# Optimization experiments

Measured on AMD Instinct MI355X. Metric: run time of the kernel, lower is better.

The kernel has to match this reference:

```python
import jax, jax.numpy as jnp
import numpy as np

B, C_IN, C_OUT, D, H, W = 2, 128, 128, 16, 32, 32


def setup_inputs() -> dict:
    key = jax.random.key(0)
    kx, kw, kb = jax.random.split(key, 3)
    x = jax.random.normal(kx, (B, C_IN, D, H, W), dtype=jnp.float32)
    # ddpm_conv3x3 -> Conv3d(in_ch, out_ch, kernel=3, padding=1) with default (scaled-variance) init
    fan_in = C_IN * 3 * 3 * 3
    scale = 1.0 / np.sqrt(fan_in)
    Wk = jax.random.uniform(kw, (C_OUT, C_IN, 3, 3, 3), dtype=jnp.float32, minval=-scale, maxval=scale)
    b = jnp.zeros((C_OUT,), dtype=jnp.float32)
    return {"x": x, "Wk": Wk, "b": b}


def reference(x, Wk, b):
    h = jnp.repeat(jnp.repeat(jnp.repeat(x, 2, axis=2), 2, axis=3), 2, axis=4)
    # 3x3x3 conv, stride 1, padding 1 (SAME)
    out = jax.lax.conv_general_dilated(
        h, Wk,
        window_strides=(1, 1, 1),
        padding="SAME",
        dimension_numbers=("NCDHW", "OIDHW", "NCDHW"),
    )
    return out + b[None, :, None, None, None]
```

## Files before the change

kernel.cpp:

```cpp
#include <hip/hip_runtime.h>
#include <hip/hip_bf16.h>

#define B_    2
#define CIN   128
#define COUT  128
#define DD    16
#define HH    32
#define WW    32
#define XS_CI (DD*HH*WW)
#define XS_B  (CIN*XS_CI)
#define OS_H2 64
#define OS_D2 (64*64)
#define OS_CO (32*64*64)
#define OS_B  (COUT*OS_CO)

#define PD_D  18
#define PD_H  34
#define PD_W  36
#define PD_HW (PD_H*PD_W)
#define PD_CI (PD_D*PD_HW)
#define AFOLD_BYTES (8*32*8*64*16)
#define XPAD_ELEMS  ((size_t)B_*CIN*PD_CI)
#define XPAD_BYTES  (XPAD_ELEMS*2)

typedef __attribute__((ext_vector_type(8))) short        short8;
typedef __attribute__((ext_vector_type(4))) float        floatx4;
typedef __attribute__((ext_vector_type(4))) unsigned int uint4v;

static __device__ __forceinline__ unsigned f2bf(float f) {
    union { __hip_bfloat16 h; unsigned short u; } cv;
    cv.h = __float2bfloat16(f);
    return (unsigned)cv.u;
}

__global__ __launch_bounds__(256) void fold_kernel(const float* __restrict__ Wk,
                                                   unsigned short* __restrict__ Afold) {
    const int t = blockIdx.x * 256 + threadIdx.x;
    const int p  = t >> 14;
    const int ks = (t >> 9) & 31;
    const int ct = (t >> 6) & 7;
    const int l  = t & 63;
    const int co = ct * 16 + (l & 15);
    const int ci = ks * 4 + (l >> 4);
    const int ed = (p >> 2) & 1, eh = (p >> 1) & 1, ew = p & 1;

    const float* w = Wk + (co * CIN + ci) * 27;
    float wv[27];
    #pragma unroll
    for (int i = 0; i < 27; ++i) wv[i] = w[i];

    short8 pk;
    #pragma unroll
    for (int tt = 0; tt < 8; ++tt) {
        const int td = (tt >> 2) & 1, th = (tt >> 1) & 1, tw = tt & 1;
        const int dlo = ed ? (td ? 2 : 0) : (td ? 1 : 0);
        const int dhi = ed ? (td ? 2 : 1) : (td ? 2 : 0);
        const int hlo = eh ? (th ? 2 : 0) : (th ? 1 : 0);
        const int hhi = eh ? (th ? 2 : 1) : (th ? 2 : 0);
        const int wlo = ew ? (tw ? 2 : 0) : (tw ? 1 : 0);
        const int whi = ew ? (tw ? 2 : 1) : (tw ? 2 : 0);
        float s = 0.f;
        for (int kd = dlo; kd <= dhi; ++kd)
            for (int kh = hlo; kh <= hhi; ++kh)
                for (int kw = wlo; kw <= whi; ++kw)
                    s += wv[kd * 9 + kh * 3 + kw];
        pk[tt] = (short)f2bf(s);
    }
    reinterpret_cast<short8*>(Afold)[t] = pk;
}

__global__ __launch_bounds__(256) void pad_kernel(const float* __restrict__ x,
                                                  unsigned* __restrict__ xp32) {
    const int idx = blockIdx.x * 256 + threadIdx.x;
    const int w2 = idx & 15;
    const int h  = (idx >> 4) & 31;
    const int d  = (idx >> 9) & 15;
    const int ci = (idx >> 13) & 127;
    const int b  = (idx >> 20) & 1;
    const float2 v = *reinterpret_cast<const float2*>(
        x + (size_t)((b * CIN + ci) * DD + d) * (HH * WW) + h * WW + w2 * 2);
    xp32[(size_t)((b * CIN + ci) * PD_D + d + 1) * (PD_HW / 2)
         + (h + 1) * (PD_W / 2) + (w2 + 1)] = f2bf(v.x) | (f2bf(v.y) << 16);
}

__global__ __launch_bounds__(256, 3) void upconv_mfma(
    const unsigned short* __restrict__ xp,
    const unsigned short* __restrict__ Afold,
    const float* __restrict__ bias,
    float* __restrict__ out)
{
    __shared__ short Bt[2][128 * 64];
    char* buf0 = reinterpret_cast<char*>(&Bt[0][0]);
    char* buf1 = reinterpret_cast<char*>(&Bt[1][0]);

    const int tid  = threadIdx.x;
    const int wave = tid >> 6;
    const int lane = tid & 63;

    const int d      = blockIdx.x >> 3;
    const int h_base = (blockIdx.x & 7) * 4;
    const int p      = blockIdx.y;
    const int b      = blockIdx.z;
    const int ed = (p >> 2) & 1, eh = (p >> 1) & 1, ew = p & 1;

    const int npair = tid & 63;
    const int grp   = tid >> 6;
    const int hl    = npair >> 4;
    const int wlp   = (npair & 15) * 2;
    const int n_a   = hl * 32 + wlp;
    const int n_b   = n_a + 1;
    const int pd  = d + ed;
    const int ph  = h_base + hl + eh;
    const int pwb = wlp + 2 * ew;
    const int roff = pd * PD_HW + ph * PD_W + pwb;
    const unsigned short* xpb = xp + (size_t)b * CIN * PD_CI;

    int waddr_a[2], waddr_b[2];
    #pragma unroll
    for (int i = 0; i < 2; ++i) {
        const int cl = grp * 2 + i;
        waddr_a[i] = n_a * 128 + ((cl * 16) ^ (((n_a >> 1) & 7) << 4));
        waddr_b[i] = n_b * 128 + ((cl * 16) ^ (((n_b >> 1) & 7) << 4));
    }

    const int co0 = (wave >> 1) * 64;
    const int n0  = (wave & 1) * 64;
    const int ct0 = (wave >> 1) * 4;
    int raddr[2][4];
    #pragma unroll
    for (int ksl = 0; ksl < 2; ++ksl)
        #pragma unroll
        for (int nt = 0; nt < 4; ++nt) {
            const int n  = n0 + nt * 16 + (lane & 15);
            const int kb = ksl * 64 + (lane >> 4) * 16;
            raddr[ksl][nt] = n * 128 + (kb ^ (((n >> 1) & 7) << 4));
        }

    floatx4 acc[4][4];
    #pragma unroll
    for (int i = 0; i < 4; ++i)
        #pragma unroll
        for (int j = 0; j < 4; ++j)
            acc[i][j] = (floatx4){0.f, 0.f, 0.f, 0.f};

    const short8* Ap = reinterpret_cast<const short8*>(Afold);

    unsigned gA[2][4][2], gB[2][4][2];

    #define GATHER(gbuf, kc)                                                    \
        do {                                                                    \
            _Pragma("unroll")                                                   \
            for (int i = 0; i < 2; ++i) {                                       \
                const char* bc = reinterpret_cast<const char*>(                 \
                    xpb + (size_t)((kc) * 8 + grp * 2 + i) * PD_CI + roff);     \
                gbuf[i][0][0] = *(const unsigned*)(bc + 0);                     \
                gbuf[i][0][1] = *(const unsigned*)(bc + 4);                     \
                gbuf[i][1][0] = *(const unsigned*)(bc + 72);                    \
                gbuf[i][1][1] = *(const unsigned*)(bc + 76);                    \
                gbuf[i][2][0] = *(const unsigned*)(bc + 2448);                  \
                gbuf[i][2][1] = *(const unsigned*)(bc + 2452);                  \
                gbuf[i][3][0] = *(const unsigned*)(bc + 2520);                  \
                gbuf[i][3][1] = *(const unsigned*)(bc + 2524);                  \
            }                                                                   \
        } while (0)

    #define BODY(kc, bufc, g, dofill)                                           \
        do {                                                                    \
                                   \
            short8 a[2][4];                                                     \
            _Pragma("unroll")                                                   \
            for (int ksl = 0; ksl < 2; ++ksl)                                   \
                _Pragma("unroll")                                               \
                for (int ct = 0; ct < 4; ++ct)                                  \
                    a[ksl][ct] = Ap[(size_t)(((p) * 32 + (kc) * 2 + ksl) * 8    \
                                             + ct0 + ct) * 64 + lane];          \
                    \
            _Pragma("unroll")                                                   \
            for (int i = 0; i < 2; ++i) {                                       \
                unsigned pa[4], pb[4];                                          \
                _Pragma("unroll")                                               \
                for (int r = 0; r < 4; ++r) {                                   \
                    const unsigned l0 = g[i][r][0], l1 = g[i][r][1];            \
                    const unsigned mid = (l0 >> 16) | (l1 << 16);               \
                    pa[r] = ew ? l0  : mid;                                     \
                    pb[r] = ew ? mid : l1;                                      \
                }                                                               \
                *(uint4v*)(bufc + waddr_a[i]) = (uint4v){pa[0],pa[1],pa[2],pa[3]}; \
                *(uint4v*)(bufc + waddr_b[i]) = (uint4v){pb[0],pb[1],pb[2],pb[3]}; \
            }                                                                   \
               \
            if (dofill) GATHER(g, (kc) + 2);                                    \
                       \
            asm volatile("s_waitcnt lgkmcnt(0)\n\ts_barrier" ::: "memory");     \
                                                                   \
            __builtin_amdgcn_s_setprio(1);                                      \
            _Pragma("unroll")                                                   \
            for (int ksl = 0; ksl < 2; ++ksl) {                                 \
                short8 bfr[4];                                                  \
                _Pragma("unroll")                                               \
                for (int nt = 0; nt < 4; ++nt)                                  \
                    bfr[nt] = *reinterpret_cast<const short8*>(                 \
                        bufc + raddr[ksl][nt]);                                 \
                _Pragma("unroll")                                               \
                for (int ct = 0; ct < 4; ++ct)                                  \
                    _Pragma("unroll")                                           \
                    for (int nt = 0; nt < 4; ++nt)                              \
                        acc[ct][nt] = __builtin_amdgcn_mfma_f32_16x16x32_bf16(  \
                            a[ksl][ct], bfr[nt], acc[ct][nt], 0, 0, 0);         \
            }                                                                   \
            __builtin_amdgcn_s_setprio(0);                                      \
        } while (0)

    GATHER(gA, 0);
    GATHER(gB, 1);
    for (int kc = 0; kc < 16; kc += 2) {
        BODY(kc,     buf0, gA, kc + 2 < 16);
        BODY(kc + 1, buf1, gB, kc + 3 < 16);
    }
    #undef BODY
    #undef GATHER

    float* ob = out + (size_t)b * OS_B + (size_t)(2 * d + ed) * OS_D2;
    #pragma unroll
    for (int ct = 0; ct < 4; ++ct) {
        #pragma unroll
        for (int j = 0; j < 4; ++j) {
            const int co = co0 + ct * 16 + (lane >> 4) * 4 + j;
            const float bv = bias[co];
            #pragma unroll
            for (int nt = 0; nt < 4; ++nt) {
                const int n  = n0 + nt * 16 + (lane & 15);
                const int hh = n >> 5, wl = n & 31;
                const int h2 = 2 * (h_base + hh) + eh;
                const int w2 = 2 * wl + ew;
                ob[(size_t)co * OS_CO + h2 * OS_H2 + w2] = acc[ct][nt][j] + bv;
            }
        }
    }
}

extern "C" void kernel_launch(void* const* d_in, const int* in_sizes, int n_in,
                              void* d_out, int out_size, void* d_ws, size_t ws_size,
                              hipStream_t stream) {
    const float* x    = (const float*)d_in[0];
    const float* Wk   = (const float*)d_in[1];
    const float* bias = (const float*)d_in[2];
    float* out        = (float*)d_out;

    unsigned short* Afold = (unsigned short*)d_ws;
    unsigned short* xpad  = (unsigned short*)((char*)d_ws + AFOLD_BYTES);

    hipMemsetAsync(xpad, 0, XPAD_BYTES, stream);
    pad_kernel<<<8192, 256, 0, stream>>>(x, (unsigned*)xpad);
    fold_kernel<<<512, 256, 0, stream>>>(Wk, Afold);

    dim3 grid(DD * 8, 8, B_);
    upconv_mfma<<<grid, 256, 0, stream>>>(xpad, Afold, bias, out);
}
```

Before: 131.7 us.

## Stage input tiles via global_load_lds with pre-shifted odd-aligned input copy

Builds a second, one-element-shifted bf16 copy of the padded input so every gathered dword is aligned, then loads B-operand tiles straight into LDS with global_load_lds instead of through registers and ds_write. The main loop is re-pipelined with vmcnt-based waits and explicit barriers around double buffers. This targets the register staging, shift/select ALU work and LDS write traffic in the conv loop. In exchange it adds an extra pre-pass kernel, doubles the padded-input workspace, issues many 4-byte direct loads, and adds a second barrier per iteration.

```diff
diff --git a/kernel.cpp b/kernel.cpp
--- a/kernel.cpp
+++ b/kernel.cpp
@@ -7,8 +7,6 @@
 #define DD    16
 #define HH    32
 #define WW    32
-#define XS_CI (DD*HH*WW)
-#define XS_B  (CIN*XS_CI)
 #define OS_H2 64
 #define OS_D2 (64*64)
 #define OS_CO (32*64*64)
@@ -16,16 +14,16 @@
 
 #define PD_D  18
 #define PD_H  34
-#define PD_W  36
-#define PD_HW (PD_H*PD_W)
-#define PD_CI (PD_D*PD_HW)
+#define RD    18
+#define HWD   (PD_H*RD)
+#define CID   (PD_D*HWD)
+#define CI8B  (8*CID*4)
+#define ARRD  ((size_t)B_*CIN*CID)
+#define ARRB  ((int)(ARRD*4))
 #define AFOLD_BYTES (8*32*8*64*16)
-#define XPAD_ELEMS  ((size_t)B_*CIN*PD_CI)
-#define XPAD_BYTES  (XPAD_ELEMS*2)
-
-typedef __attribute__((ext_vector_type(8))) short        short8;
-typedef __attribute__((ext_vector_type(4))) float        floatx4;
-typedef __attribute__((ext_vector_type(4))) unsigned int uint4v;
+
+typedef __attribute__((ext_vector_type(8))) short  short8;
+typedef __attribute__((ext_vector_type(4))) float  floatx4;
 
 static __device__ __forceinline__ unsigned f2bf(float f) {
     union { __hip_bfloat16 h; unsigned short u; } cv;
@@ -70,7 +68,7 @@
 }
 
 __global__ __launch_bounds__(256) void pad_kernel(const float* __restrict__ x,
-                                                  unsigned* __restrict__ xp32) {
+                                                  unsigned* __restrict__ xe) {
     const int idx = blockIdx.x * 256 + threadIdx.x;
     const int w2 = idx & 15;
     const int h  = (idx >> 4) & 31;
@@ -79,12 +77,20 @@
     const int b  = (idx >> 20) & 1;
     const float2 v = *reinterpret_cast<const float2*>(
         x + (size_t)((b * CIN + ci) * DD + d) * (HH * WW) + h * WW + w2 * 2);
-    xp32[(size_t)((b * CIN + ci) * PD_D + d + 1) * (PD_HW / 2)
-         + (h + 1) * (PD_W / 2) + (w2 + 1)] = f2bf(v.x) | (f2bf(v.y) << 16);
+    xe[(size_t)((b * CIN + ci) * PD_D + d + 1) * HWD
+       + (h + 1) * RD + (w2 + 1)] = f2bf(v.x) | (f2bf(v.y) << 16);
+}
+
+__global__ __launch_bounds__(256) void xo_kernel(const unsigned* __restrict__ xe,
+                                                 unsigned* __restrict__ xo) {
+    const size_t t = (size_t)blockIdx.x * 256 + threadIdx.x;
+    const unsigned e0 = xe[t];
+    const unsigned e1 = (t + 1 < ARRD) ? xe[t + 1] : 0u;
+    xo[t] = (e0 >> 16) | (e1 << 16);
 }
 
 __global__ __launch_bounds__(256, 3) void upconv_mfma(
-    const unsigned short* __restrict__ xp,
+    const char* __restrict__ xps,
     const unsigned short* __restrict__ Afold,
     const float* __restrict__ bias,
     float* __restrict__ out)
@@ -103,25 +109,23 @@
     const int b      = blockIdx.z;
     const int ed = (p >> 2) & 1, eh = (p >> 1) & 1, ew = p & 1;
 
-    const int npair = tid & 63;
-    const int grp   = tid >> 6;
-    const int hl    = npair >> 4;
-    const int wlp   = (npair & 15) * 2;
-    const int n_a   = hl * 32 + wlp;
-    const int n_b   = n_a + 1;
-    const int pd  = d + ed;
-    const int ph  = h_base + hl + eh;
-    const int pwb = wlp + 2 * ew;
-    const int roff = pd * PD_HW + ph * PD_W + pwb;
-    const unsigned short* xpb = xp + (size_t)b * CIN * PD_CI;
-
-    int waddr_a[2], waddr_b[2];
-    #pragma unroll
-    for (int i = 0; i < 2; ++i) {
-        const int cl = grp * 2 + i;
-        waddr_a[i] = n_a * 128 + ((cl * 16) ^ (((n_a >> 1) & 7) << 4));
-        waddr_b[i] = n_b * 128 + ((cl * 16) ^ (((n_b >> 1) & 7) << 4));
-    }
+    const int l31 = lane & 31, l5 = lane >> 5;
+    const int colinc = (ew + l5) ? 1 : 0;
+    const int isE    = (ew + l5) & 1;
+    const int pd0 = d + ed;
+    const int ph0 = h_base + wave + eh;
+    int goff[16];
+    #pragma unroll
+    for (int i = 0; i < 16; ++i) {
+        const int kd = l31 ^ ((i & 7) << 2);
+        const int cl = kd >> 2, r = kd & 3;
+        const int dpad = pd0 + (r >> 1);
+        const int hpad = ph0 + (r & 1);
+        const int col  = i + colinc;
+        const int dword = ((b * CIN + cl) * PD_D + dpad) * HWD + hpad * RD + col;
+        goff[i] = dword * 4 + (isE ? 0 : ARRB);
+    }
+    const int wrow = wave * 32 * 128;
 
     const int co0 = (wave >> 1) * 64;
     const int n0  = (wave & 1) * 64;
@@ -145,28 +149,20 @@
 
     const short8* Ap = reinterpret_cast<const short8*>(Afold);
 
-    unsigned gA[2][4][2], gB[2][4][2];
-
-    #define GATHER(gbuf, kc)                                                    \
+    #define STAGE(nbufc)                                                        \
         do {                                                                    \
             _Pragma("unroll")                                                   \
-            for (int i = 0; i < 2; ++i) {                                       \
-                const char* bc = reinterpret_cast<const char*>(                 \
-                    xpb + (size_t)((kc) * 8 + grp * 2 + i) * PD_CI + roff);     \
-                gbuf[i][0][0] = *(const unsigned*)(bc + 0);                     \
-                gbuf[i][0][1] = *(const unsigned*)(bc + 4);                     \
-                gbuf[i][1][0] = *(const unsigned*)(bc + 72);                    \
-                gbuf[i][1][1] = *(const unsigned*)(bc + 76);                    \
-                gbuf[i][2][0] = *(const unsigned*)(bc + 2448);                  \
-                gbuf[i][2][1] = *(const unsigned*)(bc + 2452);                  \
-                gbuf[i][3][0] = *(const unsigned*)(bc + 2520);                  \
-                gbuf[i][3][1] = *(const unsigned*)(bc + 2524);                  \
+            for (int i = 0; i < 16; ++i) {                                      \
+                __builtin_amdgcn_global_load_lds(                               \
+                    (const __attribute__((address_space(1))) void*)(xps + goff[i]), \
+                    (__attribute__((address_space(3))) void*)((nbufc) + wrow + i * 256), \
+                    4, 0, 0);                                                   \
+                goff[i] += CI8B;                                                \
             }                                                                   \
         } while (0)
 
-    #define BODY(kc, bufc, g, dofill)                                           \
+    #define BODYM(kc, bufc, nbufc, DO_STAGE, VMCNT_STR)                         \
         do {                                                                    \
-                                   \
             short8 a[2][4];                                                     \
             _Pragma("unroll")                                                   \
             for (int ksl = 0; ksl < 2; ++ksl)                                   \
@@ -174,25 +170,10 @@
                 for (int ct = 0; ct < 4; ++ct)                                  \
                     a[ksl][ct] = Ap[(size_t)(((p) * 32 + (kc) * 2 + ksl) * 8    \
                                              + ct0 + ct) * 64 + lane];          \
-                    \
-            _Pragma("unroll")                                                   \
-            for (int i = 0; i < 2; ++i) {                                       \
-                unsigned pa[4], pb[4];                                          \
-                _Pragma("unroll")                                               \
-                for (int r = 0; r < 4; ++r) {                                   \
-                    const unsigned l0 = g[i][r][0], l1 = g[i][r][1];            \
-                    const unsigned mid = (l0 >> 16) | (l1 << 16);               \
-                    pa[r] = ew ? l0  : mid;                                     \
-                    pb[r] = ew ? mid : l1;                                      \
-                }                                                               \
-                *(uint4v*)(bufc + waddr_a[i]) = (uint4v){pa[0],pa[1],pa[2],pa[3]}; \
-                *(uint4v*)(bufc + waddr_b[i]) = (uint4v){pb[0],pb[1],pb[2],pb[3]}; \
-            }                                                                   \
-               \
-            if (dofill) GATHER(g, (kc) + 2);                                    \
-                       \
-            asm volatile("s_waitcnt lgkmcnt(0)\n\ts_barrier" ::: "memory");     \
-                                                                   \
+            if (DO_STAGE) STAGE(nbufc);                                         \
+            asm volatile(VMCNT_STR ::: "memory");                               \
+            __builtin_amdgcn_sched_barrier(0);                                  \
+            __builtin_amdgcn_s_barrier();                                       \
             __builtin_amdgcn_s_setprio(1);                                      \
             _Pragma("unroll")                                                   \
             for (int ksl = 0; ksl < 2; ++ksl) {                                 \
@@ -200,7 +181,7 @@
                 _Pragma("unroll")                                               \
                 for (int nt = 0; nt < 4; ++nt)                                  \
                     bfr[nt] = *reinterpret_cast<const short8*>(                 \
-                        bufc + raddr[ksl][nt]);                                 \
+                        (bufc) + raddr[ksl][nt]);                               \
                 _Pragma("unroll")                                               \
                 for (int ct = 0; ct < 4; ++ct)                                  \
                     _Pragma("unroll")                                           \
@@ -209,16 +190,20 @@
                             a[ksl][ct], bfr[nt], acc[ct][nt], 0, 0, 0);         \
             }                                                                   \
             __builtin_amdgcn_s_setprio(0);                                      \
+            __builtin_amdgcn_sched_barrier(0);                                  \
+            __builtin_amdgcn_s_barrier();                                       \
+            __builtin_amdgcn_sched_barrier(0);                                  \
         } while (0)
 
-    GATHER(gA, 0);
-    GATHER(gB, 1);
-    for (int kc = 0; kc < 16; kc += 2) {
-        BODY(kc,     buf0, gA, kc + 2 < 16);
-        BODY(kc + 1, buf1, gB, kc + 3 < 16);
-    }
-    #undef BODY
-    #undef GATHER
+    STAGE(buf0);
+    for (int kc = 0; kc < 14; kc += 2) {
+        BODYM(kc,     buf0, buf1, 1, "s_waitcnt vmcnt(24)");
+        BODYM(kc + 1, buf1, buf0, 1, "s_waitcnt vmcnt(24)");
+    }
+    BODYM(14, buf0, buf1, 1, "s_waitcnt vmcnt(24)");
+    BODYM(15, buf1, buf0, 0, "s_waitcnt vmcnt(8)");
+    #undef BODYM
+    #undef STAGE
 
     float* ob = out + (size_t)b * OS_B + (size_t)(2 * d + ed) * OS_D2;
     #pragma unroll
@@ -248,12 +233,15 @@
     float* out        = (float*)d_out;
 
     unsigned short* Afold = (unsigned short*)d_ws;
-    unsigned short* xpad  = (unsigned short*)((char*)d_ws + AFOLD_BYTES);
-
-    hipMemsetAsync(xpad, 0, XPAD_BYTES, stream);
-    pad_kernel<<<8192, 256, 0, stream>>>(x, (unsigned*)xpad);
+    char* xe = (char*)d_ws + AFOLD_BYTES;
+    char* xo = xe + ARRB;
+
+    hipMemsetAsync(xe, 0, (size_t)2 * ARRB, stream);
+    pad_kernel<<<8192, 256, 0, stream>>>(x, (unsigned*)xe);
+    xo_kernel<<<(unsigned)(ARRD / 256), 256, 0, stream>>>((const unsigned*)xe,
+                                                          (unsigned*)xo);
     fold_kernel<<<512, 256, 0, stream>>>(Wk, Afold);
 
     dim3 grid(DD * 8, 8, B_);
-    upconv_mfma<<<grid, 256, 0, stream>>>(xpad, Afold, bias, out);
-}
+    upconv_mfma<<<grid, 256, 0, stream>>>(xe, Afold, bias, out);
+}
```

After: 285.4 us. +116.8%, slower.
